# Kernel tuning notes

Hardware: AMD Instinct MI355X
Metric: run time of the kernel (lower is better)

Reference implementation:

```python
import jax, jax.numpy as jnp
import numpy as np


def _lstm1_step(x, Wih, bih, bhh):
    # nn.LSTM applied to a length-1 sequence with zero initial (h, c):
    # h_prev = 0 so W_hh contributes 0; c = sigmoid(i)*tanh(g); h = sigmoid(o)*tanh(c).
    gates = x @ Wih.T + bih + bhh            # (..., 4H), torch gate order i,f,g,o
    i, f, g, o = jnp.split(gates, 4, axis=-1)
    c = jax.nn.sigmoid(i) * jnp.tanh(g)
    return jax.nn.sigmoid(o) * jnp.tanh(c)


def _lstm2_layer(x, Wih, Whh, bih, bhh):
    # Full recurrent LSTM layer over time; x: (B, T, H) -> outputs (B, T, H).
    B = x.shape[0]
    H = Whh.shape[1]
    xg = x @ Wih.T + bih + bhh               # precompute input gates (B, T, 4H)
    def step(carry, g_t):                    # g_t: (B, 4H)
        h, c = carry
        gates = g_t + h @ Whh.T
        i, f, g, o = jnp.split(gates, 4, axis=-1)
        c = jax.nn.sigmoid(f) * c + jax.nn.sigmoid(i) * jnp.tanh(g)
        h = jax.nn.sigmoid(o) * jnp.tanh(c)
        return (h, c), h
    h0 = jnp.zeros((B, H), x.dtype)
    _, hs = jax.lax.scan(step, (h0, h0), jnp.swapaxes(xg, 0, 1))
    return jnp.swapaxes(hs, 0, 1)            # (B, T, H)


def setup_inputs() -> dict:
    D, H, B, T = 256, 1024, 64, 256
    key = jax.random.key(0)
    ks = iter(jax.random.split(key, 32))
    s = 1.0 / np.sqrt(H).astype(np.float32)
    def u(shape):
        return jax.random.uniform(next(ks), shape, jnp.float32, -s, s)
    inp = {"xx": jax.random.normal(next(ks), (B, T, D), jnp.float32)}
    inp.update(
        l1_Wih0=u((4 * H, D)), l1_bih0=u((4 * H,)), l1_bhh0=u((4 * H,)),
        l1_Wih1=u((4 * H, H)), l1_bih1=u((4 * H,)), l1_bhh1=u((4 * H,)),
        l2_Wih0=u((4 * H, H)), l2_Whh0=u((4 * H, H)), l2_bih0=u((4 * H,)), l2_bhh0=u((4 * H,)),
        l2_Wih1=u((4 * H, H)), l2_Whh1=u((4 * H, H)), l2_bih1=u((4 * H,)), l2_bhh1=u((4 * H,)),
        mlp_W1=u((H, H)), mlp_b1=u((H,)),
        mlp_W2=u((H // 2, H)), mlp_b2=u((H // 2,)),
        mlp_W3=u((1, H // 2)), mlp_b3=u((1,)),
    )
    return inp


def reference(xx, l1_Wih0, l1_bih0, l1_bhh0, l1_Wih1, l1_bih1, l1_bhh1,
              l2_Wih0, l2_Whh0, l2_bih0, l2_bhh0, l2_Wih1, l2_Whh1, l2_bih1, l2_bhh1,
              mlp_W1, mlp_b1, mlp_W2, mlp_b2, mlp_W3, mlp_b3):
    # lstm1: per-timestep single-step stacked LSTM cell with zero state (vectorized over B,T)
    h = _lstm1_step(xx, l1_Wih0, l1_bih0, l1_bhh0)
    h = _lstm1_step(h, l1_Wih1, l1_bih1, l1_bhh1)          # (B, T, H) == lsout
    # lstm2: true 2-layer recurrence over T
    h = _lstm2_layer(h, l2_Wih0, l2_Whh0, l2_bih0, l2_bhh0)
    h = _lstm2_layer(h, l2_Wih1, l2_Whh1, l2_bih1, l2_bhh1)
    last = h[:, -1, :]                                     # (B, H)
    z = jax.nn.relu(last @ mlp_W1.T + mlp_b1)
    z = jax.nn.relu(z @ mlp_W2.T + mlp_b2)
    out = z @ mlp_W3.T + mlp_b3                            # (B, 1)
    return out[:, 0]                                       # out_m: (B,)
```

## Files before the change

### kernel.cpp

```cpp
#include <hip/hip_runtime.h>

typedef unsigned short u16;
typedef unsigned int u32;
typedef u16 u16x8 __attribute__((ext_vector_type(8)));
typedef u16 u16x4 __attribute__((ext_vector_type(4)));
typedef u32 u32x4 __attribute__((ext_vector_type(4)));
typedef __bf16 bf16x8 __attribute__((ext_vector_type(8)));
typedef float f32x4 __attribute__((ext_vector_type(4)));

#define B_ 64
#define T_ 256
#define D_ 256
#define H_ 1024
#define G4 4096
#define TC 32
#define TCSH 5
#define MC 2048
#define NCHUNK 8
#define NFLG 2048

__device__ __forceinline__ u16 f2bf(float x) {
  u32 u = __builtin_bit_cast(u32, x);
  u += 0x7fffu + ((u >> 16) & 1u);
  return (u16)(u >> 16);
}
__device__ __forceinline__ float bf2f(u16 h) {
  u32 u = ((u32)h) << 16;
  return __builtin_bit_cast(float, u);
}
__device__ __forceinline__ float sigmoidf_(float x) { return 1.f / (1.f + __expf(-x)); }

__device__ __forceinline__ f32x4 mfma16(u16x8 a, u16x8 b, f32x4 c) {
  return __builtin_amdgcn_mfma_f32_16x16x32_bf16(
      __builtin_bit_cast(bf16x8, a), __builtin_bit_cast(bf16x8, b), c, 0, 0, 0);
}

__device__ __forceinline__ void gl2lds16(const u16* g, u16* l) {
  __builtin_amdgcn_global_load_lds(
      (const __attribute__((address_space(1))) u32*)(const void*)g,
      (__attribute__((address_space(3))) u32*)(void*)l, 16, 0, 0);
}

__device__ __forceinline__ void store4_cc(u16* p, u32 v) {
  asm volatile("global_store_dword %0, %1, off sc0 sc1" :: "v"(p), "v"(v) : "memory");
}
__device__ __forceinline__ void store4_cc_u32(u32* p, u32 v) {
  asm volatile("global_store_dword %0, %1, off sc0 sc1" :: "v"(p), "v"(v) : "memory");
}
__device__ __forceinline__ void store16_cc(u16* p, u32 a, u32 b, u32 c, u32 d) {
  u32x4 v = {a, b, c, d};
  asm volatile("global_store_dwordx4 %0, %1, off sc0 sc1" :: "v"(p), "v"(v) : "memory");
}
__device__ __forceinline__ void waitcnt0() {
  asm volatile("s_waitcnt vmcnt(0)" ::: "memory");
}

__global__ void k_split(const float* __restrict__ src, u16* __restrict__ hi,
                        u16* __restrict__ lo, int n4) {
  int i = blockIdx.x * 256 + threadIdx.x;
  if (i >= n4) return;
  const float4* s4 = (const float4*)src;
  float4 v = s4[i];
  u16 h0 = f2bf(v.x), h1 = f2bf(v.y), h2 = f2bf(v.z), h3 = f2bf(v.w);
  u16x4 hv = {h0, h1, h2, h3};
  u16x4 lv = {f2bf(v.x - bf2f(h0)), f2bf(v.y - bf2f(h1)),
              f2bf(v.z - bf2f(h2)), f2bf(v.w - bf2f(h3))};
  *(u16x4*)(hi + 4 * (size_t)i) = hv;
  *(u16x4*)(lo + 4 * (size_t)i) = lv;
}

__global__ void k_splitp(const float* __restrict__ src, u16* __restrict__ hi,
                         u16* __restrict__ lo, int n4, int s) {
  int i = blockIdx.x * 256 + threadIdx.x;
  if (i >= n4) return;
  int row = i >> s, col4 = i & ((1 << s) - 1);
  int g = row >> 10, u = row & 1023;
  int prow = ((u >> 4) << 6) + (g << 4) + (u & 15);
  size_t di = ((size_t)prow << s) | col4;
  const float4* s4 = (const float4*)src;
  float4 v = s4[i];
  u16 h0 = f2bf(v.x), h1 = f2bf(v.y), h2 = f2bf(v.z), h3 = f2bf(v.w);
  u16x4 hv = {h0, h1, h2, h3};
  u16x4 lv = {f2bf(v.x - bf2f(h0)), f2bf(v.y - bf2f(h1)),
              f2bf(v.z - bf2f(h2)), f2bf(v.w - bf2f(h3))};
  *(u16x4*)(hi + 4 * di) = hv;
  *(u16x4*)(lo + 4 * di) = lv;
}

__global__ void k_split_x(const float* __restrict__ xx, u16* __restrict__ hi,
                          u16* __restrict__ lo, int t0) {
  int i = blockIdx.x * 256 + threadIdx.x;
  if (i >= MC * (D_ / 4)) return;
  int row = i >> 6, c4 = i & 63;
  int b = row >> TCSH, tc = row & (TC - 1);
  const float4* s4 = (const float4*)xx;
  float4 v = s4[(size_t)(b * T_ + t0 + tc) * (D_ / 4) + c4];
  u16 h0 = f2bf(v.x), h1 = f2bf(v.y), h2 = f2bf(v.z), h3 = f2bf(v.w);
  u16x4 hv = {h0, h1, h2, h3};
  u16x4 lv = {f2bf(v.x - bf2f(h0)), f2bf(v.y - bf2f(h1)),
              f2bf(v.z - bf2f(h2)), f2bf(v.w - bf2f(h3))};
  *(u16x4*)(hi + 4 * (size_t)i) = hv;
  *(u16x4*)(lo + 4 * (size_t)i) = lv;
}

__global__ void k_addvec(const float* __restrict__ a, const float* __restrict__ b,
                         float* __restrict__ o, int n) {
  int i = blockIdx.x * 256 + threadIdx.x;
  if (i < n) o[i] = a[i] + b[i];
}

__global__ void k_addp(const float* __restrict__ a, const float* __restrict__ b,
                       float* __restrict__ o) {
  int i = blockIdx.x * 256 + threadIdx.x;
  if (i >= G4) return;
  int g = i >> 10, u = i & 1023;
  int prow = ((u >> 4) << 6) + (g << 4) + (u & 15);
  o[prow] = a[i] + b[i];
}

__global__ __launch_bounds__(256, 2) void k_gemm3(
    const u16* __restrict__ Ah, const u16* __restrict__ Al,
    const u16* __restrict__ Bh, const u16* __restrict__ Bl,
    const float* __restrict__ bias, float* __restrict__ C,
    u16* __restrict__ Hh, u16* __restrict__ Hl,
    int M, int N, int K, int rec)
{
  __shared__ __attribute__((aligned(16))) u16 sAh[2][4096];
  __shared__ __attribute__((aligned(16))) u16 sAl[2][4096];
  __shared__ __attribute__((aligned(16))) u16 sBh[2][4096];
  __shared__ __attribute__((aligned(16))) u16 sBl[2][4096];

  const int tid = threadIdx.x;
  const int lane = tid & 63;
  const int wv = tid >> 6;
  const int wm = wv & 1, wn = wv >> 1;
  const int m0 = blockIdx.x * 128;
  const int n0 = blockIdx.y * 128;

  const int r0 = tid >> 2;
  const int kg = (tid & 3) ^ (r0 & 3);
  const size_t aoff0 = (size_t)(m0 + r0) * K + kg * 8;
  const size_t aoff1 = (size_t)(m0 + r0 + 64) * K + kg * 8;
  const size_t boff0 = (size_t)(n0 + r0) * K + kg * 8;
  const size_t boff1 = (size_t)(n0 + r0 + 64) * K + kg * 8;
  const int lb0 = wv * 512;
  const int lb1 = 2048 + wv * 512;

  const int l15 = lane & 15, l4 = lane >> 4;
  int afo[4], bfo[4];
#pragma unroll
  for (int mt = 0; mt < 4; ++mt) {
    int r = wm * 64 + mt * 16 + l15;
    afo[mt] = (r * 4 + (l4 ^ (r & 3))) * 8;
  }
#pragma unroll
  for (int nt = 0; nt < 4; ++nt) {
    int r = wn * 64 + nt * 16 + l15;
    bfo[nt] = (r * 4 + (l4 ^ (r & 3))) * 8;
  }

#define STAGE_G(bi, kk) do { \
    gl2lds16(Ah + aoff0 + (kk), &sAh[bi][lb0]); \
    gl2lds16(Ah + aoff1 + (kk), &sAh[bi][lb1]); \
    gl2lds16(Al + aoff0 + (kk), &sAl[bi][lb0]); \
    gl2lds16(Al + aoff1 + (kk), &sAl[bi][lb1]); \
    gl2lds16(Bh + boff0 + (kk), &sBh[bi][lb0]); \
    gl2lds16(Bh + boff1 + (kk), &sBh[bi][lb1]); \
    gl2lds16(Bl + boff0 + (kk), &sBl[bi][lb0]); \
    gl2lds16(Bl + boff1 + (kk), &sBl[bi][lb1]); \
  } while (0)

  f32x4 acc[4][4] = {};

  STAGE_G(0, 0);
  __syncthreads();

  int cur = 0;
  for (int k0 = 0; k0 < K; k0 += 32) {
    if (k0 + 32 < K) STAGE_G(cur ^ 1, k0 + 32);

    u16x8 a_h[4], a_l[4], b_h[4], b_l[4];
#pragma unroll
    for (int i = 0; i < 4; ++i) {
      a_h[i] = *(const u16x8*)&sAh[cur][afo[i]];
      a_l[i] = *(const u16x8*)&sAl[cur][afo[i]];
      b_h[i] = *(const u16x8*)&sBh[cur][bfo[i]];
      b_l[i] = *(const u16x8*)&sBl[cur][bfo[i]];
    }
#pragma unroll
    for (int mt = 0; mt < 4; ++mt)
#pragma unroll
      for (int nt = 0; nt < 4; ++nt) {
        acc[mt][nt] = mfma16(a_h[mt], b_h[nt], acc[mt][nt]);
        acc[mt][nt] = mfma16(a_l[mt], b_h[nt], acc[mt][nt]);
        acc[mt][nt] = mfma16(a_h[mt], b_l[nt], acc[mt][nt]);
      }

    __syncthreads();
    cur ^= 1;
  }
#undef STAGE_G

  if (rec == 0) {
#pragma unroll
    for (int mt = 0; mt < 4; ++mt) {
      int mr = m0 + wm * 64 + mt * 16 + l4 * 4;
#pragma unroll
      for (int nt = 0; nt < 4; ++nt) {
        int nc = n0 + wn * 64 + nt * 16 + l15;
        float bv = bias[nc];
#pragma unroll
        for (int r = 0; r < 4; ++r)
          C[(size_t)(mr + r) * N + nc] = acc[mt][nt][r] + bv;
      }
    }
  } else if (rec == 3) {
    const int cb = n0 + wn * 64;
    const int ub = (cb >> 6) * 16 + l15;
    const float bvi = bias[cb + l15];
    const float bvg = bias[cb + 32 + l15];
    const float bvo = bias[cb + 48 + l15];
#pragma unroll
    for (int mt = 0; mt < 4; ++mt) {
      int mr = m0 + wm * 64 + mt * 16 + l4 * 4;
#pragma unroll
      for (int r = 0; r < 4; ++r) {
        float gi = acc[mt][0][r] + bvi;
        float gg = acc[mt][2][r] + bvg;
        float go = acc[mt][3][r] + bvo;
        float cc2 = sigmoidf_(gi) * tanhf(gg);
        float h = sigmoidf_(go) * tanhf(cc2);
        u16 hh = f2bf(h);
        size_t oi = (size_t)(mr + r) * 1024 + ub;
        Hh[oi] = hh;
        Hl[oi] = f2bf(h - bf2f(hh));
      }
    }
  } else {
#pragma unroll
    for (int mt = 0; mt < 4; ++mt) {
      int mr = m0 + wm * 64 + mt * 16 + l4 * 4;
#pragma unroll
      for (int nt = 0; nt < 4; ++nt) {
        int nc = n0 + wn * 64 + nt * 16 + l15;
        float bv = bias[nc];
        int unit = nc & 1023;
        int ublk = unit >> 3;
        int uu = unit & 7;
        int gate = nc >> 10;
#pragma unroll
        for (int r = 0; r < 4; ++r) {
          int m = mr + r;
          int tq = (rec == 1) ? (m & (TC - 1)) : (m >> 6);
          int bq = (rec == 1) ? (m >> TCSH) : (m & 63);
          size_t idx = ((size_t)(ublk * TC + tq) * 4 + gate) * 512 + bq * 8 + uu;
          C[idx] = acc[mt][nt][r] + bv;
        }
      }
    }
  }
}

__global__ __launch_bounds__(512, 2) void k_recd(
    const float* __restrict__ xgA, const float* __restrict__ xgB,
    const u16* __restrict__ WAhi, const u16* __restrict__ WAlo,
    const u16* __restrict__ WBhi, const u16* __restrict__ WBlo,
    u16* __restrict__ rAH, u16* __restrict__ rAL,
    u16* __restrict__ rBH, u16* __restrict__ rBL,
    u16* __restrict__ cAH, u16* __restrict__ cAL,
    u16* __restrict__ cBH, u16* __restrict__ cBL,
    float* __restrict__ cbA, float* __restrict__ cbB,
    float* __restrict__ hfB,
    u32* __restrict__ flags)
{
  __shared__ __attribute__((aligned(16))) u16 sW[66048];
  __shared__ float sg[2][64][34];
  __shared__ int sDead;

  const int tid = threadIdx.x;
  const int lane = tid & 63, wv = tid >> 6;
  const int l15 = lane & 15, l4 = lane >> 4;
  const int L = blockIdx.x >> 7, ublk = blockIdx.x & 127;
  const int u0 = ublk * 8;

  const float* xg = L ? xgB : xgA;
  if (!xg) return;
  const u16* Whi = L ? WBhi : WAhi;
  const u16* Wlo = L ? WBlo : WAlo;
  u16* ringH = L ? rBH : rAH;
  u16* ringL = L ? rBL : rAL;
  u16* carryH = L ? cBH : cAH;
  u16* carryL = L ? cBL : cAL;
  float* cbp = L ? cbB : cbA;
  float* hfinal = L ? hfB : nullptr;
  u32* flg = flags + L * 1024;

  if (tid == 0) sDead = 0;

  for (int ci = tid; ci < 8192; ci += 512) {
    int plane = ci >> 12, rem = ci & 4095;
    int n = rem >> 7, ch = rem & 127;
    int wrow = (n >> 3) * 1024 + u0 + (n & 7);
    const u16* src = (plane ? Wlo : Whi) + (size_t)wrow * 1024 + ch * 8;
    gl2lds16(src, &sW[plane * 33024 + n * 1032 + ch * 8]);
  }
  __syncthreads();

  const int mt = wv >> 1, kh = wv & 1;
  const int aoff = (mt * 16 + l15) * 1024 + kh * 512 + l4 * 8;
  const int bof0 = l15 * 1032 + kh * 512 + l4 * 8;
  const int bof1 = (16 + l15) * 1032 + kh * 512 + l4 * 8;

  const u32* f0a = flg + (2 * mt) * 128 + kh * 64 + lane;
  const u32* f0b = flg + (2 * mt + 1) * 128 + kh * 64 + lane;
  u32* fown = flg + wv * 128 + ublk;

  const int pb = tid >> 3, uu = tid & 7;
  const int cidx = pb * 1024 + u0 + uu;
  float c = cbp[cidx];
  const float* xgb = xg + (size_t)ublk * (TC * 2048) + pb * 8 + uu;

  for (int t = 0; t < TC; ++t) {
    float px0, px1, px2, px3;
    {
      const float* xa = xgb + (size_t)t * 2048;
      asm volatile("global_load_dword %0, %1, off" : "=v"(px0) : "v"(xa));
      asm volatile("global_load_dword %0, %1, off" : "=v"(px1) : "v"(xa + 512));
      asm volatile("global_load_dword %0, %1, off" : "=v"(px2) : "v"(xa + 1024));
      asm volatile("global_load_dword %0, %1, off" : "=v"(px3) : "v"(xa + 1536));
    }

    if (t > 0 && *(volatile int*)&sDead == 0) {
      int guard = 0;
      for (;;) {
        u32 a = __hip_atomic_load(f0a, __ATOMIC_RELAXED, __HIP_MEMORY_SCOPE_AGENT);
        u32 b = __hip_atomic_load(f0b, __ATOMIC_RELAXED, __HIP_MEMORY_SCOPE_AGENT);
        if (a >= (u32)t && b >= (u32)t) break;
        if (++guard > (1 << 17)) { if (lane == 0) sDead = 1; break; }
        __builtin_amdgcn_s_sleep(1);
      }
    }

    const u16* oah = (t ? ringH + (size_t)(t - 1) * 65536 : carryH) + aoff;
    const u16* oal = (t ? ringL + (size_t)(t - 1) * 65536 : carryL) + aoff;
    u16x8 oh[16], ol[16];
#pragma unroll
    for (int kc = 0; kc < 16; ++kc) {
      oh[kc] = *(const u16x8*)(oah + kc * 32);
      ol[kc] = *(const u16x8*)(oal + kc * 32);
    }
    f32x4 aq[2][2] = {};
#pragma unroll
    for (int kc = 0; kc < 16; ++kc) {
      const int ko = kc * 32;
      u16x8 b0h = *(const u16x8*)&sW[bof0 + ko];
      u16x8 b0l = *(const u16x8*)&sW[33024 + bof0 + ko];
      u16x8 b1h = *(const u16x8*)&sW[bof1 + ko];
      u16x8 b1l = *(const u16x8*)&sW[33024 + bof1 + ko];
      aq[0][kc & 1] = mfma16(oh[kc], b0h, aq[0][kc & 1]);
      aq[0][kc & 1] = mfma16(ol[kc], b0h, aq[0][kc & 1]);
      aq[0][kc & 1] = mfma16(oh[kc], b0l, aq[0][kc & 1]);
      aq[1][kc & 1] = mfma16(oh[kc], b1h, aq[1][kc & 1]);
      aq[1][kc & 1] = mfma16(ol[kc], b1h, aq[1][kc & 1]);
      aq[1][kc & 1] = mfma16(oh[kc], b1l, aq[1][kc & 1]);
    }
    f32x4 A0 = aq[0][0] + aq[0][1];
    f32x4 A1 = aq[1][0] + aq[1][1];

    __syncthreads();
#pragma unroll
    for (int r4 = 0; r4 < 4; ++r4) {
      int m = mt * 16 + l4 * 4 + r4;
      sg[kh][m][l15] = A0[r4];
      sg[kh][m][16 + l15] = A1[r4];
    }
    __syncthreads();

    float g0 = sg[0][pb][uu] + sg[1][pb][uu];
    float g1 = sg[0][pb][8 + uu] + sg[1][pb][8 + uu];
    float g2 = sg[0][pb][16 + uu] + sg[1][pb][16 + uu];
    float g3 = sg[0][pb][24 + uu] + sg[1][pb][24 + uu];
    waitcnt0();
    g0 += px0; g1 += px1; g2 += px2; g3 += px3;
    c = sigmoidf_(g1) * c + sigmoidf_(g0) * tanhf(g2);
    float h = sigmoidf_(g3) * tanhf(c);
    u32 hiu = (u32)f2bf(h);
    u32 lou = (u32)f2bf(h - bf2f((u16)hiu));
    u32 pH = hiu | (__shfl_down(hiu, 1) << 16);
    u32 pL = lou | (__shfl_down(lou, 1) << 16);
    u32 qH1 = __shfl_down(pH, 2), qH2 = __shfl_down(pH, 4), qH3 = __shfl_down(pH, 6);
    u32 qL1 = __shfl_down(pL, 2), qL2 = __shfl_down(pL, 4), qL3 = __shfl_down(pL, 6);
    if ((tid & 7) == 0) {
      size_t re = (size_t)t * 65536 + (size_t)pb * 1024 + u0;
      store16_cc(ringH + re, pH, qH1, qH2, qH3);
      store16_cc(ringL + re, pL, qL1, qL2, qL3);
      if (t == TC - 1) {
        size_t ce = (size_t)pb * 1024 + u0;
        store16_cc(carryH + ce, pH, qH1, qH2, qH3);
        store16_cc(carryL + ce, pL, qL1, qL2, qL3);
      }
    }
    if (hfinal && t == TC - 1) hfinal[cidx] = h;

    waitcnt0();
    if (lane == 0) store4_cc_u32(fown, (u32)(t + 1));
  }

  cbp[cidx] = c;
}

__global__ void k_fc(const float* __restrict__ in, const float* __restrict__ W,
                     const float* __restrict__ bias, float* __restrict__ out,
                     int K, int N, int relu) {
  int b = blockIdx.x;
  int n = blockIdx.y * 256 + threadIdx.x;
  if (n >= N) return;
  const float4* wr = (const float4*)(W + (size_t)n * K);
  const float4* xr = (const float4*)(in + (size_t)b * K);
  float s = 0.f;
  for (int k = 0; k < K / 4; ++k) {
    float4 w = wr[k], x = xr[k];
    s += w.x * x.x + w.y * x.y + w.z * x.z + w.w * x.w;
  }
  s += bias[n];
  if (relu) s = fmaxf(s, 0.f);
  out[(size_t)b * N + n] = s;
}

__global__ void k_out(const float* __restrict__ z, const float* __restrict__ W3,
                      const float* __restrict__ b3, float* __restrict__ outp) {
  int b = blockIdx.x;
  int lane = threadIdx.x;
  const float4* wr = (const float4*)W3;
  const float4* xr = (const float4*)(z + b * 512);
  float s = 0.f;
  for (int k = lane; k < 128; k += 64) {
    float4 w = wr[k], x = xr[k];
    s += w.x * x.x + w.y * x.y + w.z * x.z + w.w * x.w;
  }
  for (int off = 32; off; off >>= 1) s += __shfl_down(s, off);
  if (lane == 0) outp[b] = s + b3[0];
}

extern "C" void kernel_launch(void* const* d_in, const int* in_sizes, int n_in,
                              void* d_out, int out_size, void* d_ws, size_t ws_size,
                              hipStream_t stream) {
  (void)in_sizes; (void)n_in; (void)out_size; (void)ws_size;
  const float* xx  = (const float*)d_in[0];
  const float* W10 = (const float*)d_in[1];
  const float* b10i = (const float*)d_in[2];
  const float* b10h = (const float*)d_in[3];
  const float* W11 = (const float*)d_in[4];
  const float* b11i = (const float*)d_in[5];
  const float* b11h = (const float*)d_in[6];
  const float* W20 = (const float*)d_in[7];
  const float* Wh0 = (const float*)d_in[8];
  const float* b20i = (const float*)d_in[9];
  const float* b20h = (const float*)d_in[10];
  const float* W21 = (const float*)d_in[11];
  const float* Wh1 = (const float*)d_in[12];
  const float* b21i = (const float*)d_in[13];
  const float* b21h = (const float*)d_in[14];
  const float* mW1 = (const float*)d_in[15];
  const float* mb1 = (const float*)d_in[16];
  const float* mW2 = (const float*)d_in[17];
  const float* mb2 = (const float*)d_in[18];
  const float* mW3 = (const float*)d_in[19];
  const float* mb3 = (const float*)d_in[20];

  char* ws = (char*)d_ws;
  size_t o = 0;
  float* XG0 = (float*)(ws + o); o += (size_t)MC * G4 * 4;
  float* XG1 = (float*)(ws + o); o += (size_t)MC * G4 * 4;
  u16* Aah = (u16*)(ws + o); o += (size_t)MC * H_ * 2;
  u16* Aal = (u16*)(ws + o); o += (size_t)MC * H_ * 2;
  u16* Abh = (u16*)(ws + o); o += (size_t)MC * H_ * 2;
  u16* Abl = (u16*)(ws + o); o += (size_t)MC * H_ * 2;
  u16* XXh = (u16*)(ws + o); o += (size_t)MC * D_ * 2;
  u16* XXl = (u16*)(ws + o); o += (size_t)MC * D_ * 2;
  u16* W10h = (u16*)(ws + o); o += (size_t)G4 * D_ * 2;
  u16* W10l = (u16*)(ws + o); o += (size_t)G4 * D_ * 2;
  u16* W11h = (u16*)(ws + o); o += (size_t)G4 * H_ * 2;
  u16* W11l = (u16*)(ws + o); o += (size_t)G4 * H_ * 2;
  u16* W20h = (u16*)(ws + o); o += (size_t)G4 * H_ * 2;
  u16* W20l = (u16*)(ws + o); o += (size_t)G4 * H_ * 2;
  u16* Wh0h = (u16*)(ws + o); o += (size_t)G4 * H_ * 2;
  u16* Wh0l = (u16*)(ws + o); o += (size_t)G4 * H_ * 2;
  u16* W21h = (u16*)(ws + o); o += (size_t)G4 * H_ * 2;
  u16* W21l = (u16*)(ws + o); o += (size_t)G4 * H_ * 2;
  u16* Wh1h = (u16*)(ws + o); o += (size_t)G4 * H_ * 2;
  u16* Wh1l = (u16*)(ws + o); o += (size_t)G4 * H_ * 2;
  float* bs0 = (float*)(ws + o); o += G4 * 4;
  float* bs1 = (float*)(ws + o); o += G4 * 4;
  float* bs2 = (float*)(ws + o); o += G4 * 4;
  float* bs3 = (float*)(ws + o); o += G4 * 4;
  char* ST = ws + o;
  u16* h00H = (u16*)(ws + o); o += B_ * H_ * 2;
  u16* h00L = (u16*)(ws + o); o += B_ * H_ * 2;
  u16* h01H = (u16*)(ws + o); o += B_ * H_ * 2;
  u16* h01L = (u16*)(ws + o); o += B_ * H_ * 2;
  float* cb0 = (float*)(ws + o); o += B_ * H_ * 4;
  float* cb1 = (float*)(ws + o); o += B_ * H_ * 4;
  u32* FLG = (u32*)(ws + o); o += (NCHUNK + 1) * NFLG * 4;
  size_t stBytes = (size_t)((ws + o) - ST);
  float* FH = (float*)(ws + o); o += B_ * H_ * 4;
  float* Z1 = (float*)(ws + o); o += B_ * H_ * 4;
  float* Z2 = (float*)(ws + o); o += B_ * 512 * 4;

  u16 *r0H = Abh, *r0L = Abl, *r1H = Aah, *r1L = Aal;

  k_splitp<<<(G4 * D_ / 4 + 255) / 256, 256, 0, stream>>>(W10, W10h, W10l, G4 * D_ / 4, 6);
  k_splitp<<<(G4 * H_ / 4 + 255) / 256, 256, 0, stream>>>(W11, W11h, W11l, G4 * H_ / 4, 8);
  k_split<<<(G4 * H_ / 4 + 255) / 256, 256, 0, stream>>>(W20, W20h, W20l, G4 * H_ / 4);
  k_split<<<(G4 * H_ / 4 + 255) / 256, 256, 0, stream>>>(Wh0, Wh0h, Wh0l, G4 * H_ / 4);
  k_split<<<(G4 * H_ / 4 + 255) / 256, 256, 0, stream>>>(W21, W21h, W21l, G4 * H_ / 4);
  k_split<<<(G4 * H_ / 4 + 255) / 256, 256, 0, stream>>>(Wh1, Wh1h, Wh1l, G4 * H_ / 4);
  k_addp<<<16, 256, 0, stream>>>(b10i, b10h, bs0);
  k_addp<<<16, 256, 0, stream>>>(b11i, b11h, bs1);
  k_addvec<<<16, 256, 0, stream>>>(b20i, b20h, bs2, G4);
  k_addvec<<<16, 256, 0, stream>>>(b21i, b21h, bs3, G4);
  hipMemsetAsync(ST, 0, stBytes, stream);

  dim3 gg(MC / 128, G4 / 128);

  for (int c = 0; c < NCHUNK; ++c) {
    int t0 = c * TC;
    k_split_x<<<(MC * (D_ / 4) + 255) / 256, 256, 0, stream>>>(xx, XXh, XXl, t0);
    k_gemm3<<<gg, 256, 0, stream>>>(XXh, XXl, W10h, W10l, bs0, nullptr,
                                    Aah, Aal, MC, G4, D_, 3);
    k_gemm3<<<gg, 256, 0, stream>>>(Aah, Aal, W11h, W11l, bs1, nullptr,
                                    Abh, Abl, MC, G4, H_, 3);
    k_gemm3<<<gg, 256, 0, stream>>>(Abh, Abl, W20h, W20l, bs2, XG0,
                                    nullptr, nullptr, MC, G4, H_, 1);
    k_recd<<<256, 512, 0, stream>>>(XG0, (c > 0) ? XG1 : nullptr,
                                    Wh0h, Wh0l, Wh1h, Wh1l,
                                    r0H, r0L, r1H, r1L,
                                    h00H, h00L, h01H, h01L, cb0, cb1,
                                    nullptr, FLG + c * NFLG);
    k_gemm3<<<gg, 256, 0, stream>>>(r0H, r0L, W21h, W21l, bs3, XG1,
                                    nullptr, nullptr, MC, G4, H_, 2);
  }
  k_recd<<<256, 512, 0, stream>>>(nullptr, XG1,
                                  Wh0h, Wh0l, Wh1h, Wh1l,
                                  r0H, r0L, r1H, r1L,
                                  h00H, h00L, h01H, h01L, cb0, cb1,
                                  FH, FLG + NCHUNK * NFLG);

  k_fc<<<dim3(B_, 4), 256, 0, stream>>>(FH, mW1, mb1, Z1, H_, H_, 1);
  k_fc<<<dim3(B_, 2), 256, 0, stream>>>(Z1, mW2, mb2, Z2, H_, 512, 1);
  k_out<<<B_, 64, 0, stream>>>(Z2, mW3, mb3, (float*)d_out);
}
```

Baseline: 4.489 ms.

## Enlarge split-bf16 GEMM tiles to 256x256 with 512-thread blocks

Replaces the 128x128 three-pass bf16 GEMM with a 256x256 tile computed by 8 waves, each owning a 128x64 sub-tile. Loads of A fragments are streamed per m-tile instead of held all at once. The goal is to cut global/LDS traffic per FLOP through higher reuse. In exchange the grid shrinks to 128 blocks, fewer than the CU count, and the LDS footprint doubles, which limits occupancy.

After: 5.393 ms. 20.1% more time.

```diff
diff --git a/kernel.cpp b/kernel.cpp
--- a/kernel.cpp
+++ b/kernel.cpp
@@ -118,39 +118,42 @@
   o[prow] = a[i] + b[i];
 }
 
-__global__ __launch_bounds__(256, 2) void k_gemm3(
+__global__ __launch_bounds__(512, 2) void k_gemm256(
     const u16* __restrict__ Ah, const u16* __restrict__ Al,
     const u16* __restrict__ Bh, const u16* __restrict__ Bl,
     const float* __restrict__ bias, float* __restrict__ C,
     u16* __restrict__ Hh, u16* __restrict__ Hl,
     int M, int N, int K, int rec)
 {
-  __shared__ __attribute__((aligned(16))) u16 sAh[2][4096];
-  __shared__ __attribute__((aligned(16))) u16 sAl[2][4096];
-  __shared__ __attribute__((aligned(16))) u16 sBh[2][4096];
-  __shared__ __attribute__((aligned(16))) u16 sBl[2][4096];
+  __shared__ __attribute__((aligned(16))) u16 sAh[2][8192];
+  __shared__ __attribute__((aligned(16))) u16 sAl[2][8192];
+  __shared__ __attribute__((aligned(16))) u16 sBh[2][8192];
+  __shared__ __attribute__((aligned(16))) u16 sBl[2][8192];
 
   const int tid = threadIdx.x;
   const int lane = tid & 63;
   const int wv = tid >> 6;
   const int wm = wv & 1, wn = wv >> 1;
-  const int m0 = blockIdx.x * 128;
-  const int n0 = blockIdx.y * 128;
-
-  const int r0 = tid >> 2;
-  const int kg = (tid & 3) ^ (r0 & 3);
-  const size_t aoff0 = (size_t)(m0 + r0) * K + kg * 8;
-  const size_t aoff1 = (size_t)(m0 + r0 + 64) * K + kg * 8;
-  const size_t boff0 = (size_t)(n0 + r0) * K + kg * 8;
-  const size_t boff1 = (size_t)(n0 + r0 + 64) * K + kg * 8;
-  const int lb0 = wv * 512;
-  const int lb1 = 2048 + wv * 512;
+  const int m0 = blockIdx.x * 256;
+  const int n0 = blockIdx.y * 256;
+
+  const int rl = lane >> 2;
+  const int cg = lane & 3;
+  const int row0 = wv * 32 + rl;
+  const int row1 = wv * 32 + 16 + rl;
+  const int kofs = (cg ^ (rl & 3)) * 8;
+  const size_t aS0 = (size_t)(m0 + row0) * K + kofs;
+  const size_t aS1 = (size_t)(m0 + row1) * K + kofs;
+  const size_t bS0 = (size_t)(n0 + row0) * K + kofs;
+  const size_t bS1 = (size_t)(n0 + row1) * K + kofs;
+  const int ld0 = wv * 1024;
+  const int ld1 = wv * 1024 + 512;
 
   const int l15 = lane & 15, l4 = lane >> 4;
-  int afo[4], bfo[4];
-#pragma unroll
-  for (int mt = 0; mt < 4; ++mt) {
-    int r = wm * 64 + mt * 16 + l15;
+  int afo[8], bfo[4];
+#pragma unroll
+  for (int mt = 0; mt < 8; ++mt) {
+    int r = wm * 128 + mt * 16 + l15;
     afo[mt] = (r * 4 + (l4 ^ (r & 3))) * 8;
   }
 #pragma unroll
@@ -159,70 +162,58 @@
     bfo[nt] = (r * 4 + (l4 ^ (r & 3))) * 8;
   }
 
-#define STAGE_G(bi, kk) do { \
-    gl2lds16(Ah + aoff0 + (kk), &sAh[bi][lb0]); \
-    gl2lds16(Ah + aoff1 + (kk), &sAh[bi][lb1]); \
-    gl2lds16(Al + aoff0 + (kk), &sAl[bi][lb0]); \
-    gl2lds16(Al + aoff1 + (kk), &sAl[bi][lb1]); \
-    gl2lds16(Bh + boff0 + (kk), &sBh[bi][lb0]); \
-    gl2lds16(Bh + boff1 + (kk), &sBh[bi][lb1]); \
-    gl2lds16(Bl + boff0 + (kk), &sBl[bi][lb0]); \
-    gl2lds16(Bl + boff1 + (kk), &sBl[bi][lb1]); \
+#define STG(bi, kk) do { \
+    gl2lds16(Ah + aS0 + (kk), &sAh[bi][ld0]); \
+    gl2lds16(Ah + aS1 + (kk), &sAh[bi][ld1]); \
+    gl2lds16(Al + aS0 + (kk), &sAl[bi][ld0]); \
+    gl2lds16(Al + aS1 + (kk), &sAl[bi][ld1]); \
+    gl2lds16(Bh + bS0 + (kk), &sBh[bi][ld0]); \
+    gl2lds16(Bh + bS1 + (kk), &sBh[bi][ld1]); \
+    gl2lds16(Bl + bS0 + (kk), &sBl[bi][ld0]); \
+    gl2lds16(Bl + bS1 + (kk), &sBl[bi][ld1]); \
   } while (0)
 
-  f32x4 acc[4][4] = {};
-
-  STAGE_G(0, 0);
+  f32x4 acc[8][4] = {};
+
+  STG(0, 0);
   __syncthreads();
 
   int cur = 0;
   for (int k0 = 0; k0 < K; k0 += 32) {
-    if (k0 + 32 < K) STAGE_G(cur ^ 1, k0 + 32);
-
-    u16x8 a_h[4], a_l[4], b_h[4], b_l[4];
-#pragma unroll
-    for (int i = 0; i < 4; ++i) {
-      a_h[i] = *(const u16x8*)&sAh[cur][afo[i]];
-      a_l[i] = *(const u16x8*)&sAl[cur][afo[i]];
-      b_h[i] = *(const u16x8*)&sBh[cur][bfo[i]];
-      b_l[i] = *(const u16x8*)&sBl[cur][bfo[i]];
-    }
-#pragma unroll
-    for (int mt = 0; mt < 4; ++mt)
+    if (k0 + 32 < K) STG(cur ^ 1, k0 + 32);
+
+    u16x8 b_h[4], b_l[4];
+#pragma unroll
+    for (int nt = 0; nt < 4; ++nt) {
+      b_h[nt] = *(const u16x8*)&sBh[cur][bfo[nt]];
+      b_l[nt] = *(const u16x8*)&sBl[cur][bfo[nt]];
+    }
+#pragma unroll
+    for (int mt = 0; mt < 8; ++mt) {
+      u16x8 a_h = *(const u16x8*)&sAh[cur][afo[mt]];
+      u16x8 a_l = *(const u16x8*)&sAl[cur][afo[mt]];
 #pragma unroll
       for (int nt = 0; nt < 4; ++nt) {
-        acc[mt][nt] = mfma16(a_h[mt], b_h[nt], acc[mt][nt]);
-        acc[mt][nt] = mfma16(a_l[mt], b_h[nt], acc[mt][nt]);
-        acc[mt][nt] = mfma16(a_h[mt], b_l[nt], acc[mt][nt]);
+        acc[mt][nt] = mfma16(a_h, b_h[nt], acc[mt][nt]);
+        acc[mt][nt] = mfma16(a_l, b_h[nt], acc[mt][nt]);
+        acc[mt][nt] = mfma16(a_h, b_l[nt], acc[mt][nt]);
       }
+    }
 
     __syncthreads();
     cur ^= 1;
   }
-#undef STAGE_G
-
-  if (rec == 0) {
-#pragma unroll
-    for (int mt = 0; mt < 4; ++mt) {
-      int mr = m0 + wm * 64 + mt * 16 + l4 * 4;
-#pragma unroll
-      for (int nt = 0; nt < 4; ++nt) {
-        int nc = n0 + wn * 64 + nt * 16 + l15;
-        float bv = bias[nc];
-#pragma unroll
-        for (int r = 0; r < 4; ++r)
-          C[(size_t)(mr + r) * N + nc] = acc[mt][nt][r] + bv;
-      }
-    }
-  } else if (rec == 3) {
+#undef STG
+
+  if (rec == 3) {
     const int cb = n0 + wn * 64;
     const int ub = (cb >> 6) * 16 + l15;
     const float bvi = bias[cb + l15];
     const float bvg = bias[cb + 32 + l15];
     const float bvo = bias[cb + 48 + l15];
 #pragma unroll
-    for (int mt = 0; mt < 4; ++mt) {
-      int mr = m0 + wm * 64 + mt * 16 + l4 * 4;
+    for (int mt = 0; mt < 8; ++mt) {
+      int mr = m0 + wm * 128 + mt * 16 + l4 * 4;
 #pragma unroll
       for (int r = 0; r < 4; ++r) {
         float gi = acc[mt][0][r] + bvi;
@@ -238,8 +229,8 @@
     }
   } else {
 #pragma unroll
-    for (int mt = 0; mt < 4; ++mt) {
-      int mr = m0 + wm * 64 + mt * 16 + l4 * 4;
+    for (int mt = 0; mt < 8; ++mt) {
+      int mr = m0 + wm * 128 + mt * 16 + l4 * 4;
 #pragma unroll
       for (int nt = 0; nt < 4; ++nt) {
         int nc = n0 + wn * 64 + nt * 16 + l15;
@@ -521,24 +512,24 @@
   k_addvec<<<16, 256, 0, stream>>>(b21i, b21h, bs3, G4);
   hipMemsetAsync(ST, 0, stBytes, stream);
 
-  dim3 gg(MC / 128, G4 / 128);
+  dim3 gg(MC / 256, G4 / 256);
 
   for (int c = 0; c < NCHUNK; ++c) {
     int t0 = c * TC;
     k_split_x<<<(MC * (D_ / 4) + 255) / 256, 256, 0, stream>>>(xx, XXh, XXl, t0);
-    k_gemm3<<<gg, 256, 0, stream>>>(XXh, XXl, W10h, W10l, bs0, nullptr,
-                                    Aah, Aal, MC, G4, D_, 3);
-    k_gemm3<<<gg, 256, 0, stream>>>(Aah, Aal, W11h, W11l, bs1, nullptr,
-                                    Abh, Abl, MC, G4, H_, 3);
-    k_gemm3<<<gg, 256, 0, stream>>>(Abh, Abl, W20h, W20l, bs2, XG0,
-                                    nullptr, nullptr, MC, G4, H_, 1);
+    k_gemm256<<<gg, 512, 0, stream>>>(XXh, XXl, W10h, W10l, bs0, nullptr,
+                                      Aah, Aal, MC, G4, D_, 3);
+    k_gemm256<<<gg, 512, 0, stream>>>(Aah, Aal, W11h, W11l, bs1, nullptr,
+                                      Abh, Abl, MC, G4, H_, 3);
+    k_gemm256<<<gg, 512, 0, stream>>>(Abh, Abl, W20h, W20l, bs2, XG0,
+                                      nullptr, nullptr, MC, G4, H_, 1);
     k_recd<<<256, 512, 0, stream>>>(XG0, (c > 0) ? XG1 : nullptr,
                                     Wh0h, Wh0l, Wh1h, Wh1l,
                                     r0H, r0L, r1H, r1L,
                                     h00H, h00L, h01H, h01L, cb0, cb1,
                                     nullptr, FLG + c * NFLG);
-    k_gemm3<<<gg, 256, 0, stream>>>(r0H, r0L, W21h, W21l, bs3, XG1,
-                                    nullptr, nullptr, MC, G4, H_, 2);
+    k_gemm256<<<gg, 512, 0, stream>>>(r0H, r0L, W21h, W21l, bs3, XG1,
+                                      nullptr, nullptr, MC, G4, H_, 2);
   }
   k_recd<<<256, 512, 0, stream>>>(nullptr, XG1,
                                   Wh0h, Wh0l, Wh1h, Wh1l,
```
